# Kernel tuning notes

Measured on AMD Instinct MI355X. Metric: run time of the kernel, lower is better.

## Reference

```python
import jax, jax.numpy as jnp
import numpy as np
import math

T_SCALE = 99
FEAT_DIM = 400
BATCH = 2
C = 256
NH = 8
NS = 32
NSPB = 3
RATIO = 0.5
LOCAL_STEP = 33


def build_sample_mask(T=T_SCALE, ns=NS, nspb=NSPB, ratio=RATIO):
    # Vectorized port of _get_interp1d_mask. Flat layout: [time, (bin, start, end)].
    N = ns * nspb
    e_idx, s_idx = np.meshgrid(np.arange(T), np.arange(T), indexing='ij')
    valid = s_idx < e_idx
    starts_i = s_idx[valid].astype(np.int64)
    ends_i = e_idx[valid].astype(np.int64)
    starts = starts_i.astype(np.float64)
    ends = ends_i.astype(np.float64)
    center = ends - starts + 1.0
    xmin = starts - center * ratio
    plen = (ends + center * ratio) - xmin
    S = xmin[:, None] + (plen / (N - 1.0))[:, None] * np.arange(N)[None, :]  # [P, N]
    down = np.trunc(S).astype(np.int64)  # matches int(math.modf(s)[1]) (trunc toward 0)
    dec = S - down                       # can be negative when s < 0, as in the original
    up = np.ceil(S).astype(np.int64)
    bin_col = (np.arange(N) // nspb)[None, :] * (T * T) + (starts_i * T + ends_i)[:, None]
    M = np.zeros(T * ns * T * T, np.float64)
    vd = (down >= 0) & (down <= T - 1)
    np.add.at(M, (down * (ns * T * T) + bin_col)[vd], ((1.0 - dec) / nspb)[vd])
    vu = (up >= 0) & (up <= T - 1)
    np.add.at(M, (up * (ns * T * T) + bin_col)[vu], (dec / nspb)[vu])
    return M.reshape(T, ns * T * T).astype(np.float32)


def pos_ebb(scale, size):
    pos = jnp.arange(scale, dtype=jnp.float32)[:, None]
    div = jnp.exp(jnp.arange(0, size, 2, dtype=jnp.float32) * (-math.log(10000.0) / size))
    ang = pos * div
    # interleave sin (even) / cos (odd)
    return jnp.stack([jnp.sin(ang), jnp.cos(ang)], axis=-1).reshape(scale, size)


def layer_norm(x, g, b, eps=1e-5):
    mu = jnp.mean(x, -1, keepdims=True)
    var = jnp.mean((x - mu) ** 2, -1, keepdims=True)
    return (x - mu) * jax.lax.rsqrt(var + eps) * g + b


def mha(x, w_qkv, b_qkv, w_o, b_o, nh=NH):
    t, b, c = x.shape
    hd = c // nh
    q, k, v = jnp.split(x @ w_qkv.T + b_qkv, 3, axis=-1)
    q = q.reshape(t, b, nh, hd)
    k = k.reshape(t, b, nh, hd)
    v = v.reshape(t, b, nh, hd)
    att = jnp.einsum('qbhd,kbhd->bhqk', q, k) / math.sqrt(hd)
    att = jax.nn.softmax(att, axis=-1)
    o = jnp.einsum('bhqk,kbhd->qbhd', att, v).reshape(t, b, c)
    return o @ w_o.T + b_o


def encoder(x, p):
    # PyTorch post-norm TransformerEncoder (eval mode, dropout off) + final LayerNorm
    (qkv_w, qkv_b, o_w, o_b, l1_w, l1_b, l2_w, l2_b, n1_g, n1_b, n2_g, n2_b, nf_g, nf_b) = p
    for i in range(qkv_w.shape[0]):
        a = mha(x, qkv_w[i], qkv_b[i], o_w[i], o_b[i])
        x = layer_norm(x + a, n1_g[i], n1_b[i])
        f = jax.nn.relu(x @ l1_w[i].T + l1_b[i]) @ l2_w[i].T + l2_b[i]
        x = layer_norm(x + f, n2_g[i], n2_b[i])
    return layer_norm(x, nf_g, nf_b)


def conv1d(x, w, b, pad, groups=1):
    y = jax.lax.conv_general_dilated(x, w, (1,), [(pad, pad)],
                                     dimension_numbers=('NCH', 'OIH', 'NCH'),
                                     feature_group_count=groups)
    return y + b[None, :, None]


def conv2d(x, w, b, pad):
    y = jax.lax.conv_general_dilated(x, w, (1, 1), [(pad, pad), (pad, pad)],
                                     dimension_numbers=('NCHW', 'OIHW', 'NCHW'))
    return y + b[None, :, None, None]


def conv3d(x, w, b, stride):
    y = jax.lax.conv_general_dilated(x, w, stride, [(0, 0)] * 3,
                                     dimension_numbers=('NCDHW', 'OIDHW', 'NCDHW'))
    return y + b[None, :, None, None, None]


def _forward(x, cb_w, cb_b, tg_qkv_w, tg_qkv_b, tg_o_w, tg_o_b, tg_l1_w, tg_l1_b, tg_l2_w, tg_l2_b, tg_n1_g, tg_n1_b, tg_n2_g, tg_n2_b, tg_nf_g, tg_nf_b, tl_qkv_w, tl_qkv_b, tl_o_w, tl_o_b, tl_l1_w, tl_l1_b, tl_l2_w, tl_l2_b, tl_n1_g, tl_n1_b, tl_n2_g, tl_n2_b, tl_nf_g, tl_nf_b, s1_w, s1_b, s2_w, s2_b, c3_w, c3_b, p1_w, p1_b, p2_w, p2_b, p3_w, p3_b, sample_mask):
    B, _, T = x.shape
    base = jax.nn.relu(conv1d(x, cb_w, cb_b, pad=1, groups=4))  # [B,C,T]
    # local transformer on LOCAL_STEP-strided windows
    group = T // LOCAL_STEP
    tl_p = (tl_qkv_w, tl_qkv_b, tl_o_w, tl_o_b, tl_l1_w, tl_l1_b, tl_l2_w, tl_l2_b, tl_n1_g, tl_n1_b, tl_n2_g, tl_n2_b, tl_nf_g, tl_nf_b)
    feat = base.reshape(B, C, LOCAL_STEP, group).transpose(2, 3, 0, 1).reshape(LOCAL_STEP, B * group, C)
    feat = encoder(feat + pos_ebb(LOCAL_STEP, C)[:, None, :], tl_p)
    local = feat.reshape(LOCAL_STEP * group, B, C).transpose(1, 2, 0)  # [B,C,T]
    # global bidirectional transformer (shared weights, flipped second pass)
    tg_p = (tg_qkv_w, tg_qkv_b, tg_o_w, tg_o_b, tg_l1_w, tg_l1_b, tg_l2_w, tg_l2_b, tg_n1_g, tg_n1_b, tg_n2_g, tg_n2_b, tg_nf_g, tg_nf_b)
    g = base.transpose(2, 0, 1)  # [T,B,C]
    pe = pos_ebb(T, C)[:, None, :]
    f1 = encoder(g + pe, tg_p)
    f2 = encoder(g[::-1] + pe, tg_p)
    base2 = local + (f1 + f2[::-1]).transpose(1, 2, 0)  # [B,C,T]
    s = jax.nn.relu(conv1d(base2, s1_w, s1_b, pad=1, groups=4))
    start1 = jax.nn.sigmoid(conv1d(s, s2_w, s2_b, pad=0))[:, 0, :]  # [B,T]
    # boundary-matching layer: dense matmul against precomputed interp mask
    bm = jnp.matmul(base2, sample_mask).reshape(B, C, NS, T, T)
    p = jax.nn.relu(conv3d(bm, c3_w, c3_b, (NS, 1, 1)))[:, :, 0]  # [B,C,T,T]
    p = jax.nn.relu(conv2d(p, p1_w, p1_b, pad=1))
    p = jax.nn.relu(conv2d(p, p2_w, p2_b, pad=1))
    cm = jax.nn.sigmoid(conv2d(p, p3_w, p3_b, pad=0))  # [B,2,T,T]
    return cm, start1


def setup_inputs() -> dict:
    key = jax.random.key(0)
    ks = iter(jax.random.split(key, 80))
    def rnd(shape):
        return 0.02 * jax.random.normal(next(ks), shape, dtype=jnp.float32)
    inp = {'x': jax.random.normal(next(ks), (BATCH, FEAT_DIM, T_SCALE), dtype=jnp.float32)}
    inp['cb_w'] = rnd((C, FEAT_DIM // 4, 3)); inp['cb_b'] = jnp.zeros((C,), jnp.float32)
    for pre, n in (('tg', 6), ('tl', 3)):
        inp[pre + '_qkv_w'] = rnd((n, 3 * C, C)); inp[pre + '_qkv_b'] = jnp.zeros((n, 3 * C), jnp.float32)
        inp[pre + '_o_w'] = rnd((n, C, C)); inp[pre + '_o_b'] = jnp.zeros((n, C), jnp.float32)
        inp[pre + '_l1_w'] = rnd((n, 1024, C)); inp[pre + '_l1_b'] = jnp.zeros((n, 1024), jnp.float32)
        inp[pre + '_l2_w'] = rnd((n, C, 1024)); inp[pre + '_l2_b'] = jnp.zeros((n, C), jnp.float32)
        inp[pre + '_n1_g'] = jnp.ones((n, C), jnp.float32); inp[pre + '_n1_b'] = jnp.zeros((n, C), jnp.float32)
        inp[pre + '_n2_g'] = jnp.ones((n, C), jnp.float32); inp[pre + '_n2_b'] = jnp.zeros((n, C), jnp.float32)
        inp[pre + '_nf_g'] = jnp.ones((C,), jnp.float32); inp[pre + '_nf_b'] = jnp.zeros((C,), jnp.float32)
    inp['s1_w'] = rnd((C, C // 4, 3)); inp['s1_b'] = jnp.zeros((C,), jnp.float32)
    inp['s2_w'] = rnd((1, C, 1)); inp['s2_b'] = jnp.zeros((1,), jnp.float32)
    inp['c3_w'] = rnd((C, C, NS, 1, 1)); inp['c3_b'] = jnp.zeros((C,), jnp.float32)
    inp['p1_w'] = rnd((C, C, 3, 3)); inp['p1_b'] = jnp.zeros((C,), jnp.float32)
    inp['p2_w'] = rnd((C, C, 3, 3)); inp['p2_b'] = jnp.zeros((C,), jnp.float32)
    inp['p3_w'] = rnd((2, C, 1, 1)); inp['p3_b'] = jnp.zeros((2,), jnp.float32)
    inp['sample_mask'] = jnp.asarray(build_sample_mask())  # [T, NS*T*T], exact BMN interp mask
    return inp


def reference(x, cb_w, cb_b, tg_qkv_w, tg_qkv_b, tg_o_w, tg_o_b, tg_l1_w, tg_l1_b, tg_l2_w, tg_l2_b, tg_n1_g, tg_n1_b, tg_n2_g, tg_n2_b, tg_nf_g, tg_nf_b, tl_qkv_w, tl_qkv_b, tl_o_w, tl_o_b, tl_l1_w, tl_l1_b, tl_l2_w, tl_l2_b, tl_n1_g, tl_n1_b, tl_n2_g, tl_n2_b, tl_nf_g, tl_nf_b, s1_w, s1_b, s2_w, s2_b, c3_w, c3_b, p1_w, p1_b, p2_w, p2_b, p3_w, p3_b, sample_mask):
    return _forward(x, cb_w, cb_b, tg_qkv_w, tg_qkv_b, tg_o_w, tg_o_b, tg_l1_w, tg_l1_b, tg_l2_w, tg_l2_b, tg_n1_g, tg_n1_b, tg_n2_g, tg_n2_b, tg_nf_g, tg_nf_b, tl_qkv_w, tl_qkv_b, tl_o_w, tl_o_b, tl_l1_w, tl_l1_b, tl_l2_w, tl_l2_b, tl_n1_g, tl_n1_b, tl_n2_g, tl_n2_b, tl_nf_g, tl_nf_b, s1_w, s1_b, s2_w, s2_b, c3_w, c3_b, p1_w, p1_b, p2_w, p2_b, p3_w, p3_b, sample_mask)
```

## Files before the change

kernel.cpp:

```cpp
#include <hip/hip_runtime.h>
#include <math.h>

#define T99   99
#define CC    256
#define NHH   8
#define FEAT  400
#define NS_   32
#define LSTEP 33

typedef __attribute__((ext_vector_type(8))) short s8v;
typedef __attribute__((ext_vector_type(4))) float f4v;

__device__ __forceinline__ void mfma_bf16(f4v& d, s8v a, s8v b) {
  asm("v_mfma_f32_16x16x32_bf16 %0, %1, %2, %0" : "+v"(d) : "v"(a), "v"(b));
}

__device__ __forceinline__ unsigned short f2bf(float f) {
  union { float f; unsigned u; } x; x.f = f;
  unsigned r = x.u + 0x7FFFu + ((x.u >> 16) & 1u);
  return (unsigned short)(r >> 16);
}
__device__ __forceinline__ float bf2f(unsigned short h) {
  union { unsigned u; float f; } x; x.u = ((unsigned)h) << 16;
  return x.f;
}
__device__ __forceinline__ float blo(unsigned u) { union { unsigned x; float f; } c; c.x = u << 16; return c.f; }
__device__ __forceinline__ float bhi(unsigned u) { union { unsigned x; float f; } c; c.x = u & 0xffff0000u; return c.f; }

__device__ __forceinline__ float pe_val(int pos, int c) {
  int i = c >> 1;
  float freq = expf((float)(2 * i) * (-0.03597789207803197f));
  float ang = (float)pos * freq;
  return (c & 1) ? cosf(ang) : sinf(ang);
}

__global__ __launch_bounds__(128) void k_convbase(const float* __restrict__ x,
                                                  const float* __restrict__ w,
                                                  const float* __restrict__ bias,
                                                  float* __restrict__ base) {
  int b = blockIdx.x >> 8, co = blockIdx.x & 255, t = threadIdx.x;
  if (t >= T99) return;
  int g = co >> 6;
  float acc = bias[co];
  const float* xp = x + (size_t)(b * FEAT + g * 100) * T99;
  const float* wp = w + (size_t)co * 300;
  for (int ic = 0; ic < 100; ++ic) {
    float x0 = (t > 0)  ? xp[ic * T99 + t - 1] : 0.f;
    float x1 = xp[ic * T99 + t];
    float x2 = (t < 98) ? xp[ic * T99 + t + 1] : 0.f;
    acc += wp[ic * 3] * x0 + wp[ic * 3 + 1] * x1 + wp[ic * 3 + 2] * x2;
  }
  base[(size_t)(b * CC + co) * T99 + t] = fmaxf(acc, 0.f);
}

__global__ __launch_bounds__(256) void k_convW(const float* __restrict__ qkv, const float* __restrict__ o,
                                               const float* __restrict__ l1, const float* __restrict__ l2,
                                               int L, unsigned short* __restrict__ dst) {
  int total = L * 786432;
  for (int idx = blockIdx.x * 256 + threadIdx.x; idx < total; idx += gridDim.x * 256) {
    int l = idx / 786432, r = idx % 786432;
    float v;
    if (r < 196608)      v = qkv[(size_t)l * 196608 + r];
    else if (r < 262144) v = o[(size_t)l * 65536 + (r - 196608)];
    else if (r < 524288) v = l1[(size_t)l * 262144 + (r - 262144)];
    else                 v = l2[(size_t)l * 262144 + (r - 524288)];
    dst[idx] = f2bf(v);
  }
}

__global__ __launch_bounds__(256) void k_build_xg(const float* __restrict__ base, float* __restrict__ xg,
                                                  unsigned short* __restrict__ xgb) {
  int idx = blockIdx.x * 256 + threadIdx.x;
  int t = idx >> 10, r = idx & 1023, b4 = r >> 8, c = r & 255;
  float v = (b4 < 2) ? base[(size_t)(b4 * CC + c) * T99 + t]
                     : base[(size_t)((b4 - 2) * CC + c) * T99 + (98 - t)];
  v += pe_val(t, c);
  xg[idx] = v; xgb[idx] = f2bf(v);
}

__global__ __launch_bounds__(256) void k_build_xl(const float* __restrict__ base, float* __restrict__ xl,
                                                  unsigned short* __restrict__ xlb) {
  int idx = blockIdx.x * 256 + threadIdx.x;
  int ls = idx / 1536, r = idx % 1536, j = r >> 8, c = r & 255;
  int g = j >> 1, b = j & 1, t = ls * 3 + g;
  float v = base[(size_t)(b * CC + c) * T99 + t] + pe_val(ls, c);
  xl[idx] = v; xlb[idx] = f2bf(v);
}

struct GJ {
  const unsigned short* Ab;
  const unsigned short* W;
  const float* bias;
  const float* R;
  float* Yf;
  unsigned short* Yb;
  int M, N, K, flags;
};

__device__ void g_body(const GJ& j, int m0, int n0) {
  __shared__ __align__(16) unsigned short Al[64][40];
  __shared__ __align__(16) unsigned short Bl[64][40];
  int tid = threadIdx.x;
  int lane = tid & 63, w = tid >> 6, wm = w >> 1, wn = w & 1;
  int sp = tid >> 2, kc = (tid & 3) << 3;
  f4v acc[2][2];
#pragma unroll
  for (int mt = 0; mt < 2; ++mt)
#pragma unroll
    for (int nt = 0; nt < 2; ++nt) acc[mt][nt] = (f4v){0.f, 0.f, 0.f, 0.f};

  for (int k0 = 0; k0 < j.K; k0 += 32) {
    s8v av = {0, 0, 0, 0, 0, 0, 0, 0};
    int row = m0 + sp;
    if (row < j.M) av = *(const s8v*)&j.Ab[(size_t)row * j.K + k0 + kc];
    *(s8v*)&Al[sp][kc] = av;
    *(s8v*)&Bl[sp][kc] = *(const s8v*)&j.W[(size_t)(n0 + sp) * j.K + k0 + kc];
    __syncthreads();
    s8v af[2], bf[2];
#pragma unroll
    for (int mt = 0; mt < 2; ++mt)
      af[mt] = *(const s8v*)&Al[wm * 32 + mt * 16 + (lane & 15)][(lane >> 4) * 8];
#pragma unroll
    for (int nt = 0; nt < 2; ++nt)
      bf[nt] = *(const s8v*)&Bl[wn * 32 + nt * 16 + (lane & 15)][(lane >> 4) * 8];
#pragma unroll
    for (int mt = 0; mt < 2; ++mt)
#pragma unroll
      for (int nt = 0; nt < 2; ++nt) mfma_bf16(acc[mt][nt], af[mt], bf[nt]);
    __syncthreads();
  }
  asm volatile("s_nop 7\n\ts_nop 7\n\ts_nop 4");
#pragma unroll
  for (int mt = 0; mt < 2; ++mt) {
#pragma unroll
    for (int nt = 0; nt < 2; ++nt) {
      int col = n0 + wn * 32 + nt * 16 + (lane & 15);
      float bv = j.bias[col];
#pragma unroll
      for (int r = 0; r < 4; ++r) {
        int row = m0 + wm * 32 + mt * 16 + (lane >> 4) * 4 + r;
        if (row < j.M) {
          float v = acc[mt][nt][r] + bv;
          if (j.flags & 2) v += j.R[(size_t)row * j.N + col];
          if (j.flags & 1) v = fmaxf(v, 0.f);
          if (!(j.flags & 8)) j.Yf[(size_t)row * j.N + col] = v;
          if (j.flags & 4) j.Yb[(size_t)row * j.N + col] = f2bf(v);
        }
      }
    }
  }
}

__global__ __launch_bounds__(256) void k_g(GJ j) {
  if ((int)blockIdx.x * 64 >= j.M) return;
  g_body(j, blockIdx.x * 64, blockIdx.y * 64);
}

__global__ __launch_bounds__(256) void k_g2(GJ j0, GJ j1) {
  if (blockIdx.z == 0) {
    if ((int)blockIdx.x * 64 >= j0.M) return;
    g_body(j0, blockIdx.x * 64, blockIdx.y * 64);
  } else {
    if ((int)blockIdx.x * 64 >= j1.M) return;
    g_body(j1, blockIdx.x * 64, blockIdx.y * 64);
  }
}

__device__ __forceinline__ void attn_body(const unsigned short* __restrict__ qkv,
                                          unsigned short* __restrict__ attb,
                                          int T_, int B_, int bid) {
  __shared__ float qv[32];
  __shared__ float red[128];
  __shared__ float pv[128];
  int tid = threadIdx.x;
  int q = bid % T_;
  int h = (bid / T_) % NHH;
  int b = bid / (T_ * NHH);
  if (tid < 32) qv[tid] = bf2f(qkv[(size_t)(q * B_ + b) * 768 + h * 32 + tid]);
  __syncthreads();
  float s = -1e30f;
  if (tid < T_) {
    const unsigned short* kp = qkv + (size_t)(tid * B_ + b) * 768 + 256 + h * 32;
    float d = 0;
#pragma unroll
    for (int i = 0; i < 32; ++i) d += qv[i] * bf2f(kp[i]);
    s = d * 0.176776695296636881f;
  }
  red[tid] = s; __syncthreads();
  for (int o = 64; o > 0; o >>= 1) { if (tid < o) red[tid] = fmaxf(red[tid], red[tid + o]); __syncthreads(); }
  float mx = red[0]; __syncthreads();
  float p = (tid < T_) ? expf(s - mx) : 0.f;
  pv[tid] = p; red[tid] = p; __syncthreads();
  for (int o = 64; o > 0; o >>= 1) { if (tid < o) red[tid] += red[tid + o]; __syncthreads(); }
  float denom = red[0];
  __syncthreads();
  int d = tid & 31, part = tid >> 5;
  float o = 0.f;
  for (int k = part; k < T_; k += 4)
    o += pv[k] * bf2f(qkv[(size_t)(k * B_ + b) * 768 + 512 + h * 32 + d]);
  red[tid] = o; __syncthreads();
  if (tid < 32) {
    float t = red[tid] + red[tid + 32] + red[tid + 64] + red[tid + 96];
    attb[(size_t)(q * B_ + b) * 256 + h * 32 + tid] = f2bf(t / denom);
  }
}

__global__ __launch_bounds__(128) void k_attn(const unsigned short* __restrict__ qkv,
                                              unsigned short* __restrict__ attb, int T_, int B_) {
  attn_body(qkv, attb, T_, B_, blockIdx.x);
}

__global__ __launch_bounds__(128) void k_attn2(const unsigned short* __restrict__ qkv0,
                                               unsigned short* __restrict__ attb0, int T0, int B0,
                                               const unsigned short* __restrict__ qkv1,
                                               unsigned short* __restrict__ attb1, int T1, int B1) {
  int bid = blockIdx.x;
  if (blockIdx.z == 0) {
    if (bid >= B0 * NHH * T0) return;
    attn_body(qkv0, attb0, T0, B0, bid);
  } else {
    if (bid >= B1 * NHH * T1) return;
    attn_body(qkv1, attb1, T1, B1, bid);
  }
}

__device__ __forceinline__ void ln_body(const float* __restrict__ X, const float* __restrict__ g,
                                        const float* __restrict__ bb, float* __restrict__ Y,
                                        unsigned short* __restrict__ Yb, int tok) {
  __shared__ float rs[256], rq[256];
  int c = threadIdx.x;
  float v = X[(size_t)tok * 256 + c];
  rs[c] = v; rq[c] = v * v; __syncthreads();
  for (int o = 128; o > 0; o >>= 1) { if (c < o) { rs[c] += rs[c + o]; rq[c] += rq[c + o]; } __syncthreads(); }
  float mu = rs[0] * (1.f / 256.f);
  float var = rq[0] * (1.f / 256.f) - mu * mu;
  float r = (v - mu) * rsqrtf(var + 1e-5f) * g[c] + bb[c];
  Y[(size_t)tok * 256 + c] = r;
  if (Yb) Yb[(size_t)tok * 256 + c] = f2bf(r);
}

__global__ __launch_bounds__(256) void k_ln(const float* __restrict__ X, const float* __restrict__ g,
                                            const float* __restrict__ bb, float* __restrict__ Y,
                                            unsigned short* __restrict__ Yb) {
  ln_body(X, g, bb, Y, Yb, blockIdx.x);
}

__global__ __launch_bounds__(256) void k_ln2(const float* __restrict__ X0, const float* __restrict__ g0,
                                             const float* __restrict__ bb0, float* __restrict__ Y0,
                                             unsigned short* __restrict__ Yb0, int n0,
                                             const float* __restrict__ X1, const float* __restrict__ g1,
                                             const float* __restrict__ bb1, float* __restrict__ Y1,
                                             unsigned short* __restrict__ Yb1, int n1) {
  int tok = blockIdx.x;
  if (blockIdx.z == 0) { if (tok < n0) ln_body(X0, g0, bb0, Y0, Yb0, tok); }
  else                 { if (tok < n1) ln_body(X1, g1, bb1, Y1, Yb1, tok); }
}

__global__ __launch_bounds__(256) void k_combine(const float* __restrict__ encl, const float* __restrict__ encg,
                                                 float* __restrict__ base2, unsigned short* __restrict__ b2t) {
  int idx = blockIdx.x * 256 + threadIdx.x;
  int t = idx % T99, c = (idx / T99) & 255, b = idx / (CC * T99);
  int ls = t / 3, g = t % 3;
  float v = encl[(size_t)(ls * 6 + g * 2 + b) * 256 + c]
          + encg[(size_t)(t * 4 + b) * 256 + c]
          + encg[(size_t)((98 - t) * 4 + 2 + b) * 256 + c];
  base2[idx] = v;
  b2t[((size_t)(b * T99) + t) * 256 + c] = f2bf(v);
}

__global__ __launch_bounds__(256) void k_sfuse(const float* __restrict__ base2, const float* __restrict__ s1w,
                                               const float* __restrict__ s1b, const float* __restrict__ s2w,
                                               const float* __restrict__ s2b, float* __restrict__ out) {
  __shared__ float rs[256];
  int b = blockIdx.x / T99, t = blockIdx.x % T99, co = threadIdx.x;
  int g = co >> 6;
  float acc = s1b[co];
  const float* xp = base2 + (size_t)(b * CC + g * 64) * T99;
  const float* wp = s1w + (size_t)co * 192;
  for (int ic = 0; ic < 64; ++ic) {
    float x0 = (t > 0)  ? xp[ic * T99 + t - 1] : 0.f;
    float x1 = xp[ic * T99 + t];
    float x2 = (t < 98) ? xp[ic * T99 + t + 1] : 0.f;
    acc += wp[ic * 3] * x0 + wp[ic * 3 + 1] * x1 + wp[ic * 3 + 2] * x2;
  }
  rs[co] = fmaxf(acc, 0.f) * s2w[co];
  __syncthreads();
  for (int o = 128; o > 0; o >>= 1) { if (co < o) rs[co] += rs[co + o]; __syncthreads(); }
  if (co == 0) out[blockIdx.x] = 1.f / (1.f + expf(-(rs[0] + s2b[0])));
}

__global__ __launch_bounds__(256) void k_w3tb(const float* __restrict__ c3w, unsigned short* __restrict__ w3tb) {
  int idx = blockIdx.x * 256 + threadIdx.x;
  int ci = idx & 255, co = (idx >> 8) & 255, n = idx >> 16;
  w3tb[idx] = f2bf(c3w[((size_t)(co << 8) + ci) * 32 + n]);
}

__global__ __launch_bounds__(256) void k_Gm(const unsigned short* __restrict__ b2t,
                                            const unsigned short* __restrict__ w3tb,
                                            unsigned short* __restrict__ Gb) {
  __shared__ __align__(16) unsigned short Al[64][40];
  __shared__ __align__(16) unsigned short Bl[64][40];
  int nb = blockIdx.z, n = nb >> 1, b = nb & 1;
  int m0 = blockIdx.x * 64, n0 = blockIdx.y * 64;
  int tid = threadIdx.x;
  if (blockIdx.x == 0 && blockIdx.y == 0 && nb == 0)
    ((unsigned int*)(Gb + (size_t)NS_ * T99 * 512))[tid] = 0u;
  const unsigned short* A = b2t + (size_t)b * T99 * 256;
  const unsigned short* W = w3tb + (size_t)n * 65536;
  int lane = tid & 63, w = tid >> 6, wm = w >> 1, wn = w & 1;
  int sp = tid >> 2, kc = (tid & 3) << 3;
  f4v acc[2][2];
#pragma unroll
  for (int mt = 0; mt < 2; ++mt)
#pragma unroll
    for (int nt = 0; nt < 2; ++nt) acc[mt][nt] = (f4v){0.f, 0.f, 0.f, 0.f};
#pragma unroll
  for (int k0 = 0; k0 < 256; k0 += 32) {
    s8v av = {0, 0, 0, 0, 0, 0, 0, 0};
    int row = m0 + sp;
    if (row < T99) av = *(const s8v*)&A[(size_t)row * 256 + k0 + kc];
    *(s8v*)&Al[sp][kc] = av;
    *(s8v*)&Bl[sp][kc] = *(const s8v*)&W[(size_t)(n0 + sp) * 256 + k0 + kc];
    __syncthreads();
    s8v af[2], bf[2];
#pragma unroll
    for (int mt = 0; mt < 2; ++mt)
      af[mt] = *(const s8v*)&Al[wm * 32 + mt * 16 + (lane & 15)][(lane >> 4) * 8];
#pragma unroll
    for (int nt = 0; nt < 2; ++nt)
      bf[nt] = *(const s8v*)&Bl[wn * 32 + nt * 16 + (lane & 15)][(lane >> 4) * 8];
#pragma unroll
    for (int mt = 0; mt < 2; ++mt)
#pragma unroll
      for (int nt = 0; nt < 2; ++nt) mfma_bf16(acc[mt][nt], af[mt], bf[nt]);
    __syncthreads();
  }
  asm volatile("s_nop 7\n\ts_nop 7\n\ts_nop 4");
#pragma unroll
  for (int mt = 0; mt < 2; ++mt) {
#pragma unroll
    for (int nt = 0; nt < 2; ++nt) {
      int co = n0 + wn * 32 + nt * 16 + (lane & 15);
#pragma unroll
      for (int r = 0; r < 4; ++r) {
        int t = m0 + wm * 32 + mt * 16 + (lane >> 4) * 4 + r;
        if (t < T99)
          Gb[((size_t)(n * T99 + t) * 256 + co) * 2 + b] = f2bf(acc[mt][nt][r]);
      }
    }
  }
}

__global__ __launch_bounds__(256) void k_ppre(const unsigned short* __restrict__ Gb,
                                              const float* __restrict__ c3b,
                                              unsigned int* __restrict__ pinb32) {
  __shared__ float w0s[96], w1s[96];
  __shared__ int   ofs[96];
  __shared__ float part[128][4];
  int e = blockIdx.x % T99, s = blockIdx.x / T99;
  int tid = threadIdx.x;
  if (s >= e) {
    if (tid < 128) {
      float z0 = fmaxf(c3b[2 * tid], 0.f), z1 = fmaxf(c3b[2 * tid + 1], 0.f);
      unsigned int zz = ((unsigned)f2bf(z1) << 16) | (unsigned)f2bf(z0);
      pinb32[((size_t)s * T99 + e) * 128 + tid] = zz;
      pinb32[((size_t)(T99 + s) * T99 + e) * 128 + tid] = zz;
    }
    return;
  }
  if (tid < 96) {
    double center = (double)(e - s + 1);
    double S = ((double)s - 0.5 * center) + ((2.0 * center - 1.0) / 95.0) * (double)tid;
    double dn = trunc(S);
    double dec = S - dn;
    int di = (int)dn;
    double uc = ceil(S);
    int ui = (int)uc;
    int n = tid / 3;
    float w0 = 0.f, w1 = 0.f;
    int r0 = 0;
    if (dn >= 0.0 && dn <= 98.0) {
      r0 = di;
      w0 = (float)((1.0 - dec) / 3.0);
      if (uc >= 0.0 && uc <= 98.0) {
        if (ui == di) w0 += (float)(dec / 3.0);
        else          w1  = (float)(dec / 3.0);
      }
    }
    w0s[tid] = w0; w1s[tid] = w1;
    ofs[tid] = (n * T99 + r0) * 1024;
  }
  __syncthreads();
  int ch = tid & 127, half = tid >> 7;
  float a00 = 0.f, a01 = 0.f, a10 = 0.f, a11 = 0.f;
  const char* basep = (const char*)Gb + ch * 8;
  int k0 = half * 48;
#pragma unroll 8
  for (int k = k0; k < k0 + 48; ++k) {
    float w0 = w0s[k], w1 = w1s[k];
    const uint2* p = (const uint2*)(basep + ofs[k]);
    uint2 u0 = p[0];
    uint2 u1 = p[128];
    a00 += w0 * blo(u0.x) + w1 * blo(u1.x);
    a01 += w0 * bhi(u0.x) + w1 * bhi(u1.x);
    a10 += w0 * blo(u0.y) + w1 * blo(u1.y);
    a11 += w0 * bhi(u0.y) + w1 * bhi(u1.y);
  }
  if (half) { part[ch][0] = a00; part[ch][1] = a01; part[ch][2] = a10; part[ch][3] = a11; }
  __syncthreads();
  if (tid < 128) {
    a00 += part[ch][0]; a01 += part[ch][1]; a10 += part[ch][2]; a11 += part[ch][3];
    float b0 = c3b[2 * tid], b1 = c3b[2 * tid + 1];
    unsigned int zb0 = ((unsigned)f2bf(fmaxf(a10 + b1, 0.f)) << 16) | (unsigned)f2bf(fmaxf(a00 + b0, 0.f));
    unsigned int zb1 = ((unsigned)f2bf(fmaxf(a11 + b1, 0.f)) << 16) | (unsigned)f2bf(fmaxf(a01 + b0, 0.f));
    pinb32[((size_t)s * T99 + e) * 128 + tid] = zb0;
    pinb32[((size_t)(T99 + s) * T99 + e) * 128 + tid] = zb1;
  }
}

__global__ __launch_bounds__(256) void k_wb2(const float* __restrict__ pw, unsigned short* __restrict__ wbf) {
  int idx = blockIdx.x * 256 + threadIdx.x;
  if (idx >= 73728) return;
  int lane = idx & 63;
  int cog  = (idx >> 6) & 15;
  int kst  = (idx >> 10) & 7;
  int tap  = idx >> 13;
  int co = cog * 16 + (lane & 15);
  int k  = kst * 32 + (lane >> 4) * 8;
  s8v v;
#pragma unroll
  for (int j = 0; j < 8; ++j)
    v[j] = (short)f2bf(pw[((size_t)co * 256 + k + j) * 9 + tap]);
  *(s8v*)&wbf[(size_t)idx * 8] = v;
}

__global__ __launch_bounds__(256) void k_cvec(const float* __restrict__ pw, const float* __restrict__ cin,
                                              const float* __restrict__ bias, int reluCin,
                                              float* __restrict__ coutF, unsigned short* __restrict__ coutB) {
  __shared__ float rs[256];
  int co = blockIdx.x, ci = threadIdx.x;
  float c = cin[ci];
  if (reluCin) c = fmaxf(c, 0.f);
  const float* wp = pw + ((size_t)co * 256 + ci) * 9;
  float wsum = 0.f;
#pragma unroll
  for (int t = 0; t < 9; ++t) wsum += wp[t];
  rs[ci] = wsum * c;
  __syncthreads();
  for (int o = 128; o > 0; o >>= 1) { if (ci < o) rs[ci] += rs[ci + o]; __syncthreads(); }
  if (ci == 0) {
    float r = fmaxf(bias[co] + rs[0], 0.f);
    coutF[co] = r;
    coutB[co] = f2bf(r);
  }
}

__device__ __forceinline__ int aoff(int s) {
  int tap = s >> 3, kst = s & 7;
  return ((tap / 3) * 10 + (tap % 3)) * 264 + kst * 32;
}
__device__ __forceinline__ void ldb4(const unsigned short* __restrict__ B0, int s, s8v* dst) {
#pragma unroll
  for (int nt = 0; nt < 4; ++nt) dst[nt] = *(const s8v*)(B0 + (size_t)s * 8192 + nt * 512);
}

__global__ __launch_bounds__(256) void k_conv3x3(const unsigned short* __restrict__ in,
                                                 const unsigned short* __restrict__ wbf,
                                                 const float* __restrict__ bias,
                                                 const unsigned short* __restrict__ cvecB,
                                                 int D, int lo, int hi,
                                                 unsigned short* __restrict__ out) {
  __shared__ __align__(16) unsigned short Ah[100 * 264];
  int b = blockIdx.z;
  int co0 = blockIdx.y * 128;
  int ti = blockIdx.x / 13, tj = blockIdx.x % 13;
  int i0 = ti * 8, j0 = tj * 8;
  int tid = threadIdx.x;

  if (i0 - 1 >= lo && i0 + 8 <= hi && j0 - 1 >= lo && j0 + 8 <= hi && i0 - 1 >= j0 + 8 + D) {
    const unsigned int* cv = (const unsigned int*)(cvecB + co0);
    unsigned int* ob = (unsigned int*)out;
#pragma unroll
    for (int r = 0; r < 16; ++r) {
      int idx = r * 256 + tid;
      int sp = idx >> 6, cp = idx & 63;
      int gi = i0 + (sp >> 3), gj = j0 + (sp & 7);
      ob[((size_t)(b * T99 + gi) * T99 + gj) * 128 + (co0 >> 1) + cp] = cv[cp];
    }
    return;
  }

#pragma unroll
  for (int it = 0; it < 13; ++it) {
    int chunk = it * 256 + tid;
    if (chunk < 3200) {
      int row = chunk >> 5;
      int cc = (chunk & 31) * 8;
      int gi = i0 + row / 10 - 1, gj = j0 + row % 10 - 1;
      s8v val = {0, 0, 0, 0, 0, 0, 0, 0};
      if (gi >= 0 && gi < T99 && gj >= 0 && gj < T99)
        val = *(const s8v*)&in[((size_t)(b * T99 + gi) * T99 + gj) * 256 + cc];
      *(s8v*)&Ah[row * 264 + cc] = val;
    }
  }
  __syncthreads();

  int lane = tid & 63, w = tid >> 6, wm = w >> 1, wn = w & 1;
  int l15 = lane & 15, lk = lane >> 4;
  int spL0 = wm * 32 + l15, spL1 = spL0 + 16;
  int hr0 = (spL0 >> 3) * 10 + (spL0 & 7);
  int hr1 = (spL1 >> 3) * 10 + (spL1 & 7);
  const unsigned short* A0 = &Ah[hr0 * 264 + lk * 8];
  const unsigned short* A1 = &Ah[hr1 * 264 + lk * 8];
  int cogbase = blockIdx.y * 8 + wn * 4;
  const unsigned short* B0 = wbf + (size_t)cogbase * 512 + (size_t)lane * 8;

  f4v acc[2][4];
#pragma unroll
  for (int mt = 0; mt < 2; ++mt)
#pragma unroll
    for (int nt = 0; nt < 4; ++nt) acc[mt][nt] = (f4v){0.f, 0.f, 0.f, 0.f};

  s8v a0c, a1c, a0n, a1n;
  s8v bq[3][4];
  a0c = *(const s8v*)(A0 + aoff(0));
  a1c = *(const s8v*)(A1 + aoff(0));
  a0n = a0c; a1n = a1c;
  ldb4(B0, 0, bq[0]);
  ldb4(B0, 1, bq[1]);
#pragma unroll
  for (int s = 0; s < 72; ++s) {
    if (s + 2 < 72) ldb4(B0, s + 2, bq[(s + 2) % 3]);
    if (s + 1 < 72) {
      a0n = *(const s8v*)(A0 + aoff(s + 1));
      a1n = *(const s8v*)(A1 + aoff(s + 1));
    }
#pragma unroll
    for (int nt = 0; nt < 4; ++nt) {
      mfma_bf16(acc[0][nt], a0c, bq[s % 3][nt]);
      mfma_bf16(acc[1][nt], a1c, bq[s % 3][nt]);
    }
    a0c = a0n; a1c = a1n;
  }

  asm volatile("s_nop 7\n\ts_nop 7\n\ts_nop 4");
#pragma unroll
  for (int mt = 0; mt < 2; ++mt) {
#pragma unroll
    for (int nt = 0; nt < 4; ++nt) {
      int co = co0 + wn * 64 + nt * 16 + l15;
      float bv = bias[co];
#pragma unroll
      for (int r = 0; r < 4; ++r) {
        int sp = wm * 32 + mt * 16 + lk * 4 + r;
        int gi = i0 + (sp >> 3), gj = j0 + (sp & 7);
        if (gi < T99 && gj < T99) {
          float v = fmaxf(acc[mt][nt][r] + bv, 0.f);
          out[((size_t)(b * T99 + gi) * T99 + gj) * 256 + co] = f2bf(v);
        }
      }
    }
  }
}

__global__ __launch_bounds__(256) void k_p3(const unsigned short* __restrict__ p2o,
                                            const float* __restrict__ w, const float* __restrict__ bias,
                                            float* __restrict__ cm) {
  int idx = blockIdx.x * 256 + threadIdx.x;
  if (idx >= 2 * T99 * T99) return;
  int j = idx % T99, i = (idx / T99) % T99, b = idx / (T99 * T99);
  float a0 = bias[0], a1 = bias[1];
  const unsigned short* row = p2o + ((size_t)(b * T99 + i) * T99 + j) * 256;
  for (int c8 = 0; c8 < 256; c8 += 8) {
    s8v v = *(const s8v*)&row[c8];
#pragma unroll
    for (int q = 0; q < 8; ++q) {
      float x = bf2f((unsigned short)v[q]);
      a0 += w[c8 + q] * x;
      a1 += w[256 + c8 + q] * x;
    }
  }
  size_t base = (size_t)b * 2 * T99 * T99 + (size_t)i * T99 + j;
  cm[base] = 1.f / (1.f + expf(-a0));
  cm[base + T99 * T99] = 1.f / (1.f + expf(-a1));
}

struct EncW {
  const float *qkvw, *qkvb, *ow, *ob, *l1w, *l1b, *l2w, *l2b, *n1g, *n1b, *n2g, *n2b, *nfg, *nfb;
};
struct EncBufs {
  float* x; unsigned short* xb;
  float* yb;
  unsigned short *qkvb, *attb, *hb;
  int M;
};

static GJ jqkv(const EncW& W, const unsigned short* Wb, int l, const EncBufs& B) {
  GJ j = {}; j.Ab = B.xb; j.W = Wb + (size_t)l * 786432;
  j.bias = W.qkvb + (size_t)l * 768; j.Yb = B.qkvb; j.flags = 4 | 8;
  j.M = B.M; j.N = 768; j.K = 256; return j;
}
static GJ jproj(const EncW& W, const unsigned short* Wb, int l, const EncBufs& B) {
  GJ j = {}; j.Ab = B.attb; j.W = Wb + (size_t)l * 786432 + 196608;
  j.bias = W.ob + (size_t)l * 256; j.R = B.x; j.Yf = B.yb; j.flags = 2;
  j.M = B.M; j.N = 256; j.K = 256; return j;
}
static GJ jffn1(const EncW& W, const unsigned short* Wb, int l, const EncBufs& B) {
  GJ j = {}; j.Ab = B.xb; j.W = Wb + (size_t)l * 786432 + 262144;
  j.bias = W.l1b + (size_t)l * 1024; j.Yb = B.hb; j.flags = 1 | 4 | 8;
  j.M = B.M; j.N = 1024; j.K = 256; return j;
}
static GJ jffn2(const EncW& W, const unsigned short* Wb, int l, const EncBufs& B) {
  GJ j = {}; j.Ab = B.hb; j.W = Wb + (size_t)l * 786432 + 524288;
  j.bias = W.l2b + (size_t)l * 256; j.R = B.x; j.Yf = B.yb; j.flags = 2;
  j.M = B.M; j.N = 256; j.K = 1024; return j;
}

extern "C" void kernel_launch(void* const* d_in, const int* in_sizes, int n_in,
                              void* d_out, int out_size, void* d_ws, size_t ws_size,
                              hipStream_t stream) {
  (void)in_sizes; (void)n_in; (void)out_size; (void)ws_size;
  const float* x    = (const float*)d_in[0];
  const float* cbw  = (const float*)d_in[1];
  const float* cbb  = (const float*)d_in[2];
  EncW tg = {(const float*)d_in[3],  (const float*)d_in[4],  (const float*)d_in[5],  (const float*)d_in[6],
             (const float*)d_in[7],  (const float*)d_in[8],  (const float*)d_in[9],  (const float*)d_in[10],
             (const float*)d_in[11], (const float*)d_in[12], (const float*)d_in[13], (const float*)d_in[14],
             (const float*)d_in[15], (const float*)d_in[16]};
  EncW tl = {(const float*)d_in[17], (const float*)d_in[18], (const float*)d_in[19], (const float*)d_in[20],
             (const float*)d_in[21], (const float*)d_in[22], (const float*)d_in[23], (const float*)d_in[24],
             (const float*)d_in[25], (const float*)d_in[26], (const float*)d_in[27], (const float*)d_in[28],
             (const float*)d_in[29], (const float*)d_in[30]};
  const float* s1w = (const float*)d_in[31];
  const float* s1b = (const float*)d_in[32];
  const float* s2w = (const float*)d_in[33];
  const float* s2b = (const float*)d_in[34];
  const float* c3w = (const float*)d_in[35];
  const float* c3b = (const float*)d_in[36];
  const float* p1w = (const float*)d_in[37];
  const float* p1b = (const float*)d_in[38];
  const float* p2w = (const float*)d_in[39];
  const float* p2b = (const float*)d_in[40];
  const float* p3w = (const float*)d_in[41];
  const float* p3b = (const float*)d_in[42];

  float* outp = (float*)d_out;

  char* wp = (char*)d_ws;
  auto alloc = [&](size_t bytes) -> void* {
    void* p = (void*)wp;
    wp += (bytes + 255) & ~(size_t)255;
    return p;
  };
  float* base  = (float*)alloc(sizeof(float) * 2 * CC * T99);
  const int ML = 198, MG = 396;
  EncBufs BG, BL;
  BG.M = MG; BL.M = ML;
  BG.x  = (float*)alloc(sizeof(float) * MG * 256);
  BL.x  = (float*)alloc(sizeof(float) * ML * 256);
  BG.xb = (unsigned short*)alloc(sizeof(short) * MG * 256);
  BL.xb = (unsigned short*)alloc(sizeof(short) * ML * 256);
  BG.yb = (float*)alloc(sizeof(float) * MG * 256);
  BL.yb = (float*)alloc(sizeof(float) * ML * 256);
  BG.qkvb = (unsigned short*)alloc(sizeof(short) * MG * 768);
  BL.qkvb = (unsigned short*)alloc(sizeof(short) * ML * 768);
  BG.attb = (unsigned short*)alloc(sizeof(short) * MG * 256);
  BL.attb = (unsigned short*)alloc(sizeof(short) * ML * 256);
  BG.hb = (unsigned short*)alloc(sizeof(short) * MG * 1024);
  BL.hb = (unsigned short*)alloc(sizeof(short) * ML * 1024);
  float* encg  = (float*)alloc(sizeof(float) * MG * 256);
  float* encl  = (float*)alloc(sizeof(float) * ML * 256);
  float* base2 = (float*)alloc(sizeof(float) * 2 * CC * T99);
  unsigned short* b2t = (unsigned short*)alloc(sizeof(short) * 2 * T99 * 256);
  unsigned short* w3tb = (unsigned short*)alloc(sizeof(short) * 32 * 256 * 256);
  unsigned short* Gb = (unsigned short*)alloc(sizeof(short) * (2 * NS_ * T99 * 256 + 512));
  unsigned short* pinb = (unsigned short*)alloc(sizeof(short) * 2 * T99 * T99 * 256);
  unsigned short* p1o  = (unsigned short*)alloc(sizeof(short) * 2 * T99 * T99 * 256);
  unsigned short* p2o  = (unsigned short*)alloc(sizeof(short) * 2 * T99 * T99 * 256);
  unsigned short* wb2a = (unsigned short*)alloc(sizeof(short) * 9 * 256 * 256);
  unsigned short* wb2b = (unsigned short*)alloc(sizeof(short) * 9 * 256 * 256);
  unsigned short* wtgb = (unsigned short*)alloc(sizeof(short) * 6 * 786432);
  unsigned short* wtlb = (unsigned short*)alloc(sizeof(short) * 3 * 786432);
  float* c1F = (float*)alloc(sizeof(float) * 256);
  unsigned short* c1B = (unsigned short*)alloc(sizeof(short) * 256);
  float* c2F = (float*)alloc(sizeof(float) * 256);
  unsigned short* c2B = (unsigned short*)alloc(sizeof(short) * 256);

  k_convW<<<dim3(4096), dim3(256), 0, stream>>>(tg.qkvw, tg.ow, tg.l1w, tg.l2w, 6, wtgb);
  k_convW<<<dim3(2048), dim3(256), 0, stream>>>(tl.qkvw, tl.ow, tl.l1w, tl.l2w, 3, wtlb);
  k_w3tb<<<dim3(8192), dim3(256), 0, stream>>>(c3w, w3tb);
  k_wb2<<<dim3(288), dim3(256), 0, stream>>>(p1w, wb2a);
  k_wb2<<<dim3(288), dim3(256), 0, stream>>>(p2w, wb2b);
  k_cvec<<<dim3(256), dim3(256), 0, stream>>>(p1w, c3b, p1b, 1, c1F, c1B);
  k_cvec<<<dim3(256), dim3(256), 0, stream>>>(p2w, c1F, p2b, 0, c2F, c2B);
  k_convbase<<<dim3(512), dim3(128), 0, stream>>>(x, cbw, cbb, base);
  k_build_xl<<<dim3(198), dim3(256), 0, stream>>>(base, BL.x, BL.xb);
  k_build_xg<<<dim3(396), dim3(256), 0, stream>>>(base, BG.x, BG.xb);

  const int mgG = 7;
  for (int l = 0; l < 3; ++l) {
    k_g2<<<dim3(mgG, 12, 2), dim3(256), 0, stream>>>(jqkv(tl, wtlb, l, BL), jqkv(tg, wtgb, l, BG));
    k_attn2<<<dim3(4 * NHH * T99, 1, 2), dim3(128), 0, stream>>>(BL.qkvb, BL.attb, LSTEP, 6,
                                                                 BG.qkvb, BG.attb, T99, 4);
    k_g2<<<dim3(mgG, 4, 2), dim3(256), 0, stream>>>(jproj(tl, wtlb, l, BL), jproj(tg, wtgb, l, BG));
    k_ln2<<<dim3(MG, 1, 2), dim3(256), 0, stream>>>(BL.yb, tl.n1g + l * 256, tl.n1b + l * 256, BL.x, BL.xb, ML,
                                                    BG.yb, tg.n1g + l * 256, tg.n1b + l * 256, BG.x, BG.xb, MG);
    k_g2<<<dim3(mgG, 16, 2), dim3(256), 0, stream>>>(jffn1(tl, wtlb, l, BL), jffn1(tg, wtgb, l, BG));
    k_g2<<<dim3(mgG, 4, 2), dim3(256), 0, stream>>>(jffn2(tl, wtlb, l, BL), jffn2(tg, wtgb, l, BG));
    k_ln2<<<dim3(MG, 1, 2), dim3(256), 0, stream>>>(BL.yb, tl.n2g + l * 256, tl.n2b + l * 256, BL.x, BL.xb, ML,
                                                    BG.yb, tg.n2g + l * 256, tg.n2b + l * 256, BG.x, BG.xb, MG);
  }
  for (int l = 3; l < 6; ++l) {
    k_g<<<dim3(mgG, 12), dim3(256), 0, stream>>>(jqkv(tg, wtgb, l, BG));
    k_attn<<<dim3(4 * NHH * T99), dim3(128), 0, stream>>>(BG.qkvb, BG.attb, T99, 4);
    k_g<<<dim3(mgG, 4), dim3(256), 0, stream>>>(jproj(tg, wtgb, l, BG));
    k_ln<<<dim3(MG), dim3(256), 0, stream>>>(BG.yb, tg.n1g + l * 256, tg.n1b + l * 256, BG.x, BG.xb);
    k_g<<<dim3(mgG, 16), dim3(256), 0, stream>>>(jffn1(tg, wtgb, l, BG));
    k_g<<<dim3(mgG, 4), dim3(256), 0, stream>>>(jffn2(tg, wtgb, l, BG));
    k_ln<<<dim3(MG), dim3(256), 0, stream>>>(BG.yb, tg.n2g + l * 256, tg.n2b + l * 256, BG.x, BG.xb);
  }
  k_ln2<<<dim3(MG, 1, 2), dim3(256), 0, stream>>>(BL.x, tl.nfg, tl.nfb, encl, nullptr, ML,
                                                  BG.x, tg.nfg, tg.nfb, encg, nullptr, MG);
  k_combine<<<dim3(198), dim3(256), 0, stream>>>(encl, encg, base2, b2t);
  k_sfuse<<<dim3(198), dim3(256), 0, stream>>>(base2, s1w, s1b, s2w, s2b, outp + 2 * 2 * T99 * T99);
  k_Gm<<<dim3(2, 4, 64), dim3(256), 0, stream>>>(b2t, w3tb, Gb);
  k_ppre<<<dim3(T99 * T99), dim3(256), 0, stream>>>(Gb, c3b, (unsigned int*)pinb);
  k_conv3x3<<<dim3(169, 2, 2), dim3(256), 0, stream>>>(pinb, wb2a, p1b, c1B, 0, 0, 98, p1o);
  k_conv3x3<<<dim3(169, 2, 2), dim3(256), 0, stream>>>(p1o, wb2b, p2b, c2B, 2, 1, 97, p2o);
  k_p3<<<dim3(77), dim3(256), 0, stream>>>(p2o, p3w, p3b, outp);
}
```

Measured before the change: 635.4 us.

## Fuse attention, output projection, residual and LayerNorm into one per-token kernel

Replaces the per-head attention kernel, the MFMA output-projection GEMM and the LayerNorm launch with a single kernel that handles one token per block. The block computes all 8 heads, then applies a scalar fp32 projection using a new pre-transposed bf16 weight, adds the residual and normalizes. This removes two launches per layer and the round trips through the attention and projection buffers. In exchange, the projection moves from tensor-core MFMA to scalar FMAs that reread the full 256x256 weight for every token, and softmax now runs once per block per head instead of one block per query-head pair.

```diff
diff --git a/kernel.cpp b/kernel.cpp
--- a/kernel.cpp
+++ b/kernel.cpp
@@ -68,6 +68,15 @@
   }
 }
 
+__global__ __launch_bounds__(256) void k_wot(const float* __restrict__ ow, int L,
+                                             unsigned short* __restrict__ wot) {
+  int idx = blockIdx.x * 256 + threadIdx.x;
+  if (idx >= L * 65536) return;
+  int l = idx >> 16, r = idx & 65535;
+  int ci = r >> 8, co = r & 255;
+  wot[idx] = f2bf(ow[(size_t)l * 65536 + co * 256 + ci]);
+}
+
 __global__ __launch_bounds__(256) void k_build_xg(const float* __restrict__ base, float* __restrict__ xg,
                                                   unsigned short* __restrict__ xgb) {
   int idx = blockIdx.x * 256 + threadIdx.x;
@@ -166,61 +175,82 @@
   }
 }
 
-__device__ __forceinline__ void attn_body(const unsigned short* __restrict__ qkv,
-                                          unsigned short* __restrict__ attb,
-                                          int T_, int B_, int bid) {
-  __shared__ float qv[32];
-  __shared__ float red[128];
-  __shared__ float pv[128];
+__device__ void apl_body(const unsigned short* __restrict__ qkvb,
+                         const unsigned short* __restrict__ Wt,
+                         const float* __restrict__ ob,
+                         const float* __restrict__ g, const float* __restrict__ beta,
+                         float* __restrict__ X, unsigned short* __restrict__ Xb,
+                         int T_, int B_, int tok) {
+  __shared__ float qrow[256];
+  __shared__ float sc[8][100];
+  __shared__ float den[8];
+  __shared__ float att[256];
+  __shared__ float rs[256], rq[256];
   int tid = threadIdx.x;
-  int q = bid % T_;
-  int h = (bid / T_) % NHH;
-  int b = bid / (T_ * NHH);
-  if (tid < 32) qv[tid] = bf2f(qkv[(size_t)(q * B_ + b) * 768 + h * 32 + tid]);
+  int b = tok % B_;
+  qrow[tid] = bf2f(qkvb[(size_t)tok * 768 + tid]);
   __syncthreads();
-  float s = -1e30f;
-  if (tid < T_) {
-    const unsigned short* kp = qkv + (size_t)(tid * B_ + b) * 768 + 256 + h * 32;
-    float d = 0;
-#pragma unroll
-    for (int i = 0; i < 32; ++i) d += qv[i] * bf2f(kp[i]);
-    s = d * 0.176776695296636881f;
-  }
-  red[tid] = s; __syncthreads();
-  for (int o = 64; o > 0; o >>= 1) { if (tid < o) red[tid] = fmaxf(red[tid], red[tid + o]); __syncthreads(); }
-  float mx = red[0]; __syncthreads();
-  float p = (tid < T_) ? expf(s - mx) : 0.f;
-  pv[tid] = p; red[tid] = p; __syncthreads();
-  for (int o = 64; o > 0; o >>= 1) { if (tid < o) red[tid] += red[tid + o]; __syncthreads(); }
-  float denom = red[0];
+  for (int e = tid; e < 8 * T_; e += 256) {
+    int h = e / T_, k = e % T_;
+    const unsigned short* kp = qkvb + (size_t)(k * B_ + b) * 768 + 256 + h * 32;
+    float d = 0.f;
+#pragma unroll
+    for (int i = 0; i < 32; ++i) d += qrow[h * 32 + i] * bf2f(kp[i]);
+    sc[h][k] = d * 0.176776695296636881f;
+  }
   __syncthreads();
-  int d = tid & 31, part = tid >> 5;
+  int h = tid >> 5, lane = tid & 31;
+  float m = -1e30f;
+  for (int k = lane; k < T_; k += 32) m = fmaxf(m, sc[h][k]);
+#pragma unroll
+  for (int msk = 16; msk >= 1; msk >>= 1) m = fmaxf(m, __shfl_xor(m, msk, 32));
+  float sum = 0.f;
+  for (int k = lane; k < T_; k += 32) {
+    float p = expf(sc[h][k] - m);
+    sc[h][k] = p; sum += p;
+  }
+#pragma unroll
+  for (int msk = 16; msk >= 1; msk >>= 1) sum += __shfl_xor(sum, msk, 32);
+  if (lane == 0) den[h] = sum;
   float o = 0.f;
-  for (int k = part; k < T_; k += 4)
-    o += pv[k] * bf2f(qkv[(size_t)(k * B_ + b) * 768 + 512 + h * 32 + d]);
-  red[tid] = o; __syncthreads();
-  if (tid < 32) {
-    float t = red[tid] + red[tid + 32] + red[tid + 64] + red[tid + 96];
-    attb[(size_t)(q * B_ + b) * 256 + h * 32 + tid] = f2bf(t / denom);
-  }
-}
-
-__global__ __launch_bounds__(128) void k_attn(const unsigned short* __restrict__ qkv,
-                                              unsigned short* __restrict__ attb, int T_, int B_) {
-  attn_body(qkv, attb, T_, B_, blockIdx.x);
-}
-
-__global__ __launch_bounds__(128) void k_attn2(const unsigned short* __restrict__ qkv0,
-                                               unsigned short* __restrict__ attb0, int T0, int B0,
-                                               const unsigned short* __restrict__ qkv1,
-                                               unsigned short* __restrict__ attb1, int T1, int B1) {
-  int bid = blockIdx.x;
+  for (int k = 0; k < T_; ++k)
+    o += sc[h][k] * bf2f(qkvb[(size_t)(k * B_ + b) * 768 + 512 + tid]);
+  o /= den[h];
+  att[tid] = o;
+  __syncthreads();
+  float acc = ob[tid];
+#pragma unroll 8
+  for (int ci = 0; ci < 256; ++ci) acc += att[ci] * bf2f(Wt[(size_t)ci * 256 + tid]);
+  float v = acc + X[(size_t)tok * 256 + tid];
+  rs[tid] = v; rq[tid] = v * v; __syncthreads();
+  for (int oo = 128; oo > 0; oo >>= 1) { if (tid < oo) { rs[tid] += rs[tid + oo]; rq[tid] += rq[tid + oo]; } __syncthreads(); }
+  float mu = rs[0] * (1.f / 256.f);
+  float var = rq[0] * (1.f / 256.f) - mu * mu;
+  float r = (v - mu) * rsqrtf(var + 1e-5f) * g[tid] + beta[tid];
+  X[(size_t)tok * 256 + tid] = r;
+  Xb[(size_t)tok * 256 + tid] = f2bf(r);
+}
+
+__global__ __launch_bounds__(256) void k_apl(const unsigned short* qkvb, const unsigned short* Wt,
+                                             const float* ob, const float* g, const float* beta,
+                                             float* X, unsigned short* Xb, int T_, int B_, int M) {
+  if ((int)blockIdx.x >= M) return;
+  apl_body(qkvb, Wt, ob, g, beta, X, Xb, T_, B_, blockIdx.x);
+}
+
+__global__ __launch_bounds__(256) void k_apl2(const unsigned short* q0, const unsigned short* Wt0,
+                                              const float* ob0, const float* g0, const float* be0,
+                                              float* X0, unsigned short* Xb0, int T0, int B0, int M0,
+                                              const unsigned short* q1, const unsigned short* Wt1,
+                                              const float* ob1, const float* g1, const float* be1,
+                                              float* X1, unsigned short* Xb1, int T1, int B1, int M1) {
+  int tok = blockIdx.x;
   if (blockIdx.z == 0) {
-    if (bid >= B0 * NHH * T0) return;
-    attn_body(qkv0, attb0, T0, B0, bid);
+    if (tok >= M0) return;
+    apl_body(q0, Wt0, ob0, g0, be0, X0, Xb0, T0, B0, tok);
   } else {
-    if (bid >= B1 * NHH * T1) return;
-    attn_body(qkv1, attb1, T1, B1, bid);
+    if (tok >= M1) return;
+    apl_body(q1, Wt1, ob1, g1, be1, X1, Xb1, T1, B1, tok);
   }
 }
 
@@ -591,7 +621,7 @@
 struct EncBufs {
   float* x; unsigned short* xb;
   float* yb;
-  unsigned short *qkvb, *attb, *hb;
+  unsigned short *qkvb, *hb;
   int M;
 };
 
@@ -599,11 +629,6 @@
   GJ j = {}; j.Ab = B.xb; j.W = Wb + (size_t)l * 786432;
   j.bias = W.qkvb + (size_t)l * 768; j.Yb = B.qkvb; j.flags = 4 | 8;
   j.M = B.M; j.N = 768; j.K = 256; return j;
-}
-static GJ jproj(const EncW& W, const unsigned short* Wb, int l, const EncBufs& B) {
-  GJ j = {}; j.Ab = B.attb; j.W = Wb + (size_t)l * 786432 + 196608;
-  j.bias = W.ob + (size_t)l * 256; j.R = B.x; j.Yf = B.yb; j.flags = 2;
-  j.M = B.M; j.N = 256; j.K = 256; return j;
 }
 static GJ jffn1(const EncW& W, const unsigned short* Wb, int l, const EncBufs& B) {
   GJ j = {}; j.Ab = B.xb; j.W = Wb + (size_t)l * 786432 + 262144;
@@ -664,8 +689,6 @@
   BL.yb = (float*)alloc(sizeof(float) * ML * 256);
   BG.qkvb = (unsigned short*)alloc(sizeof(short) * MG * 768);
   BL.qkvb = (unsigned short*)alloc(sizeof(short) * ML * 768);
-  BG.attb = (unsigned short*)alloc(sizeof(short) * MG * 256);
-  BL.attb = (unsigned short*)alloc(sizeof(short) * ML * 256);
   BG.hb = (unsigned short*)alloc(sizeof(short) * MG * 1024);
   BL.hb = (unsigned short*)alloc(sizeof(short) * ML * 1024);
   float* encg  = (float*)alloc(sizeof(float) * MG * 256);
@@ -681,6 +704,8 @@
   unsigned short* wb2b = (unsigned short*)alloc(sizeof(short) * 9 * 256 * 256);
   unsigned short* wtgb = (unsigned short*)alloc(sizeof(short) * 6 * 786432);
   unsigned short* wtlb = (unsigned short*)alloc(sizeof(short) * 3 * 786432);
+  unsigned short* wotg = (unsigned short*)alloc(sizeof(short) * 6 * 65536);
+  unsigned short* wotl = (unsigned short*)alloc(sizeof(short) * 3 * 65536);
   float* c1F = (float*)alloc(sizeof(float) * 256);
   unsigned short* c1B = (unsigned short*)alloc(sizeof(short) * 256);
   float* c2F = (float*)alloc(sizeof(float) * 256);
@@ -688,6 +713,8 @@
 
   k_convW<<<dim3(4096), dim3(256), 0, stream>>>(tg.qkvw, tg.ow, tg.l1w, tg.l2w, 6, wtgb);
   k_convW<<<dim3(2048), dim3(256), 0, stream>>>(tl.qkvw, tl.ow, tl.l1w, tl.l2w, 3, wtlb);
+  k_wot<<<dim3(1536), dim3(256), 0, stream>>>(tg.ow, 6, wotg);
+  k_wot<<<dim3(768), dim3(256), 0, stream>>>(tl.ow, 3, wotl);
   k_w3tb<<<dim3(8192), dim3(256), 0, stream>>>(c3w, w3tb);
   k_wb2<<<dim3(288), dim3(256), 0, stream>>>(p1w, wb2a);
   k_wb2<<<dim3(288), dim3(256), 0, stream>>>(p2w, wb2b);
@@ -700,11 +727,11 @@
   const int mgG = 7;
   for (int l = 0; l < 3; ++l) {
     k_g2<<<dim3(mgG, 12, 2), dim3(256), 0, stream>>>(jqkv(tl, wtlb, l, BL), jqkv(tg, wtgb, l, BG));
-    k_attn2<<<dim3(4 * NHH * T99, 1, 2), dim3(128), 0, stream>>>(BL.qkvb, BL.attb, LSTEP, 6,
-                                                                 BG.qkvb, BG.attb, T99, 4);
-    k_g2<<<dim3(mgG, 4, 2), dim3(256), 0, stream>>>(jproj(tl, wtlb, l, BL), jproj(tg, wtgb, l, BG));
-    k_ln2<<<dim3(MG, 1, 2), dim3(256), 0, stream>>>(BL.yb, tl.n1g + l * 256, tl.n1b + l * 256, BL.x, BL.xb, ML,
-                                                    BG.yb, tg.n1g + l * 256, tg.n1b + l * 256, BG.x, BG.xb, MG);
+    k_apl2<<<dim3(MG, 1, 2), dim3(256), 0, stream>>>(
+        BL.qkvb, wotl + (size_t)l * 65536, tl.ob + l * 256, tl.n1g + l * 256, tl.n1b + l * 256,
+        BL.x, BL.xb, LSTEP, 6, ML,
+        BG.qkvb, wotg + (size_t)l * 65536, tg.ob + l * 256, tg.n1g + l * 256, tg.n1b + l * 256,
+        BG.x, BG.xb, T99, 4, MG);
     k_g2<<<dim3(mgG, 16, 2), dim3(256), 0, stream>>>(jffn1(tl, wtlb, l, BL), jffn1(tg, wtgb, l, BG));
     k_g2<<<dim3(mgG, 4, 2), dim3(256), 0, stream>>>(jffn2(tl, wtlb, l, BL), jffn2(tg, wtgb, l, BG));
     k_ln2<<<dim3(MG, 1, 2), dim3(256), 0, stream>>>(BL.yb, tl.n2g + l * 256, tl.n2b + l * 256, BL.x, BL.xb, ML,
@@ -712,9 +739,8 @@
   }
   for (int l = 3; l < 6; ++l) {
     k_g<<<dim3(mgG, 12), dim3(256), 0, stream>>>(jqkv(tg, wtgb, l, BG));
-    k_attn<<<dim3(4 * NHH * T99), dim3(128), 0, stream>>>(BG.qkvb, BG.attb, T99, 4);
-    k_g<<<dim3(mgG, 4), dim3(256), 0, stream>>>(jproj(tg, wtgb, l, BG));
-    k_ln<<<dim3(MG), dim3(256), 0, stream>>>(BG.yb, tg.n1g + l * 256, tg.n1b + l * 256, BG.x, BG.xb);
+    k_apl<<<dim3(MG), dim3(256), 0, stream>>>(BG.qkvb, wotg + (size_t)l * 65536, tg.ob + l * 256,
+                                              tg.n1g + l * 256, tg.n1b + l * 256, BG.x, BG.xb, T99, 4, MG);
     k_g<<<dim3(mgG, 16), dim3(256), 0, stream>>>(jffn1(tg, wtgb, l, BG));
     k_g<<<dim3(mgG, 4), dim3(256), 0, stream>>>(jffn2(tg, wtgb, l, BG));
     k_ln<<<dim3(MG), dim3(256), 0, stream>>>(BG.yb, tg.n2g + l * 256, tg.n2b + l * 256, BG.x, BG.xb);
```

Result: no change. 626.3 us (-1.4%).
